# Performance work log

Hardware: AMD Instinct MI355X
Metric: run time of the kernel (lower is better)

## Reference

```python
import jax, jax.numpy as jnp
import numpy as np

B, D = 4096, 1024

def setup_inputs() -> dict:
    key = jax.random.key(0)
    k1, k2, k3 = jax.random.split(key, 3)
    # q, p are row-stochastic probability distributions (original calls q.log())
    q = jax.nn.softmax(jax.random.normal(k1, (B, D), dtype=jnp.float32), axis=-1)
    p = jax.nn.softmax(jax.random.normal(k2, (B, D), dtype=jnp.float32), axis=-1)
    # binary same-class indicator matrix
    labels_matrix = jax.random.randint(k3, (B, B), 0, 2).astype(jnp.float32)
    return {"q": q, "p": p, "labels_matrix": labels_matrix}

def reference(q, p, labels_matrix):
    d = q.shape[1]
    log_q = jnp.log(q)
    log_p = jnp.log(p)
    # torch kl_div(log_q, p) = p * (log p - log q); mean over feature dim -> [B]
    kl_div = jnp.mean(p * (log_p - log_q), axis=1)
    # pairwise kl_dis[i, j] = mean_d p[j,d] * (log p[j,d] - log q[i,d])
    # = (sum_d p[j] log p[j] - (log_q @ p^T)[i, j]) / D  -- single GEMM, no BxBxD tensor
    p_entropy_term = jnp.sum(p * log_p, axis=1)          # [B]
    cross = log_q @ p.T                                   # [B, B]
    kl_dis = (p_entropy_term[None, :] - cross) / d        # [B, B]
    # original detaches kl_dis via .cpu().numpy()
    kl_dis = jax.lax.stop_gradient(kl_dis)
    positive = kl_div + jnp.sum(kl_dis * labels_matrix, axis=1)
    negative = jnp.sum(kl_dis * (1.0 - labels_matrix), axis=1)
    return jnp.sum(positive / negative)
```

## Files before the change

kernel.cpp:

```cpp
#include <hip/hip_runtime.h>
#include <hip/hip_bf16.h>
#include <stdint.h>

#define BROWS 4096
#define DDIM  1024

typedef __bf16 bf16_t;
typedef __bf16 bf16x8 __attribute__((ext_vector_type(8)));
typedef float  f32x4  __attribute__((ext_vector_type(4)));

__device__ __forceinline__ unsigned short f2bf_bits(float f) {
    union { float f; unsigned int u; } v; v.f = f;
    unsigned int u = v.u;
    unsigned int r = (u + 0x7fffu + ((u >> 16) & 1u)) >> 16;
    return (unsigned short)r;
}

__global__ __launch_bounds__(256) void prep_kernel(
    const float* __restrict__ q, const float* __restrict__ p,
    bf16_t* __restrict__ lqb, bf16_t* __restrict__ pb,
    float* __restrict__ e, float* __restrict__ kld)
{
    const int row = blockIdx.x;
    const int t   = threadIdx.x;
    const float4* q4 = (const float4*)(q + (size_t)row * DDIM);
    const float4* p4 = (const float4*)(p + (size_t)row * DDIM);
    float4 qv = q4[t];
    float4 pv = p4[t];

    float lq0 = __logf(qv.x), lq1 = __logf(qv.y), lq2 = __logf(qv.z), lq3 = __logf(qv.w);
    float lp0 = __logf(pv.x), lp1 = __logf(pv.y), lp2 = __logf(pv.z), lp3 = __logf(pv.w);

    float esum = pv.x * lp0 + pv.y * lp1 + pv.z * lp2 + pv.w * lp3;
    float ksum = pv.x * (lp0 - lq0) + pv.y * (lp1 - lq1)
               + pv.z * (lp2 - lq2) + pv.w * (lp3 - lq3);

    ushort4 uq, up;
    uq.x = f2bf_bits(lq0); uq.y = f2bf_bits(lq1); uq.z = f2bf_bits(lq2); uq.w = f2bf_bits(lq3);
    up.x = f2bf_bits(pv.x); up.y = f2bf_bits(pv.y); up.z = f2bf_bits(pv.z); up.w = f2bf_bits(pv.w);
    ((ushort4*)(lqb + (size_t)row * DDIM))[t] = uq;
    ((ushort4*)(pb  + (size_t)row * DDIM))[t] = up;

    #pragma unroll
    for (int off = 32; off > 0; off >>= 1) {
        esum += __shfl_down(esum, off);
        ksum += __shfl_down(ksum, off);
    }
    __shared__ float se[4], sk[4];
    const int wv = t >> 6, ln = t & 63;
    if (ln == 0) { se[wv] = esum; sk[wv] = ksum; }
    __syncthreads();
    if (t == 0) {
        e[row]   = se[0] + se[1] + se[2] + se[3];
        kld[row] = (sk[0] + sk[1] + sk[2] + sk[3]) * (1.0f / DDIM);
    }
}

__global__ __launch_bounds__(256) void gemm_epi_kernel(
    const bf16_t* __restrict__ Abf,
    const bf16_t* __restrict__ Bbf,
    const float*  __restrict__ L,
    const float*  __restrict__ e,
    float* __restrict__ CS, float* __restrict__ CL, float* __restrict__ EL)
{
    __shared__ bf16_t As[128 * 32];
    __shared__ bf16_t Bs[128 * 32];

    const int t    = threadIdx.x;
    const int i0   = blockIdx.y * 128;
    const int j0   = blockIdx.x * 128;
    const int wave = t >> 6;
    const int lane = t & 63;
    const int q4   = lane >> 4;
    const int ln   = lane & 15;
    const int wrow = wave >> 1;
    const int wcol = wave & 1;

    f32x4 acc[4][4];
    #pragma unroll
    for (int a = 0; a < 4; a++)
        #pragma unroll
        for (int b = 0; b < 4; b++)
            acc[a][b] = (f32x4){0.f, 0.f, 0.f, 0.f};

    const int off0 = t * 8;
    const int off1 = (t + 256) * 8;
    const int r0 = off0 >> 5, c0 = off0 & 31;
    const int r1 = off1 >> 5, c1 = off1 & 31;

    for (int k0 = 0; k0 < DDIM; k0 += 32) {
        const bf16_t* gA0 = Abf + (size_t)(i0 + r0) * DDIM + k0 + c0;
        const bf16_t* gA1 = Abf + (size_t)(i0 + r1) * DDIM + k0 + c1;
        const bf16_t* gB0 = Bbf + (size_t)(j0 + r0) * DDIM + k0 + c0;
        const bf16_t* gB1 = Bbf + (size_t)(j0 + r1) * DDIM + k0 + c1;
        __builtin_amdgcn_global_load_lds(
            (const __attribute__((address_space(1))) void*)gA0,
            (__attribute__((address_space(3))) void*)(As + off0), 16, 0, 0);
        __builtin_amdgcn_global_load_lds(
            (const __attribute__((address_space(1))) void*)gA1,
            (__attribute__((address_space(3))) void*)(As + off1), 16, 0, 0);
        __builtin_amdgcn_global_load_lds(
            (const __attribute__((address_space(1))) void*)gB0,
            (__attribute__((address_space(3))) void*)(Bs + off0), 16, 0, 0);
        __builtin_amdgcn_global_load_lds(
            (const __attribute__((address_space(1))) void*)gB1,
            (__attribute__((address_space(3))) void*)(Bs + off1), 16, 0, 0);
        __syncthreads();

        bf16x8 af[4], bfr[4];
        #pragma unroll
        for (int mi = 0; mi < 4; mi++)
            af[mi] = *(const bf16x8*)(As + (wrow * 64 + mi * 16 + ln) * 32 + q4 * 8);
        #pragma unroll
        for (int ni = 0; ni < 4; ni++)
            bfr[ni] = *(const bf16x8*)(Bs + (wcol * 64 + ni * 16 + ln) * 32 + q4 * 8);
        #pragma unroll
        for (int mi = 0; mi < 4; mi++)
            #pragma unroll
            for (int ni = 0; ni < 4; ni++)
                acc[mi][ni] = __builtin_amdgcn_mfma_f32_16x16x32_bf16(
                    af[mi], bfr[ni], acc[mi][ni], 0, 0, 0);
        __syncthreads();
    }

    const int i_base = i0 + wrow * 64;
    const int j_base = j0 + wcol * 64;

    float e_j[4];
    #pragma unroll
    for (int ni = 0; ni < 4; ni++) e_j[ni] = e[j_base + ni * 16 + ln];

    #pragma unroll
    for (int mi = 0; mi < 4; mi++) {
        #pragma unroll
        for (int r = 0; r < 4; r++) {
            const int i = i_base + mi * 16 + q4 * 4 + r;
            const float* Lrow = L + (size_t)i * BROWS + j_base;
            float cs = 0.f, cl = 0.f, el = 0.f;
            #pragma unroll
            for (int ni = 0; ni < 4; ni++) {
                float c  = acc[mi][ni][r];
                float Lv = Lrow[ni * 16 + ln];
                cs += c;
                cl += c * Lv;
                el += e_j[ni] * Lv;
            }
            #pragma unroll
            for (int s = 1; s < 16; s <<= 1) {
                cs += __shfl_xor(cs, s);
                cl += __shfl_xor(cl, s);
                el += __shfl_xor(el, s);
            }
            if (ln == 0) {
                atomicAdd(&CS[i], cs);
                atomicAdd(&CL[i], cl);
                atomicAdd(&EL[i], el);
            }
        }
    }
}

__global__ __launch_bounds__(256) void final_kernel(
    const float* __restrict__ e, const float* __restrict__ kld,
    const float* __restrict__ CS, const float* __restrict__ CL,
    const float* __restrict__ EL, float* __restrict__ out)
{
    __shared__ float sred[4];
    __shared__ float sEtot;
    const int t = threadIdx.x;

    float s = 0.f;
    for (int j = t; j < BROWS; j += 256) s += e[j];
    #pragma unroll
    for (int off = 32; off > 0; off >>= 1) s += __shfl_down(s, off);
    if ((t & 63) == 0) sred[t >> 6] = s;
    __syncthreads();
    if (t == 0) sEtot = sred[0] + sred[1] + sred[2] + sred[3];
    __syncthreads();
    const float Etot = sEtot;
    const float invD = 1.0f / DDIM;

    float rs = 0.f;
    for (int i = t; i < BROWS; i += 256) {
        float el = EL[i], cl = CL[i], cs = CS[i];
        float pos = kld[i] + (el - cl) * invD;
        float neg = (Etot - el - cs + cl) * invD;
        rs += pos / neg;
    }
    __syncthreads();
    #pragma unroll
    for (int off = 32; off > 0; off >>= 1) rs += __shfl_down(rs, off);
    if ((t & 63) == 0) sred[t >> 6] = rs;
    __syncthreads();
    if (t == 0) out[0] = sred[0] + sred[1] + sred[2] + sred[3];
}

extern "C" void kernel_launch(void* const* d_in, const int* in_sizes, int n_in,
                              void* d_out, int out_size, void* d_ws, size_t ws_size,
                              hipStream_t stream)
{
    const float* q = (const float*)d_in[0];
    const float* p = (const float*)d_in[1];
    const float* L = (const float*)d_in[2];
    float* out = (float*)d_out;

    char* ws = (char*)d_ws;
    bf16_t* lqb = (bf16_t*)ws;
    bf16_t* pb  = (bf16_t*)(ws + (size_t)BROWS * DDIM * 2);
    float*  e   = (float*)(ws + (size_t)BROWS * DDIM * 4);
    float*  kld = e + BROWS;
    float*  CS  = kld + BROWS;
    float*  CL  = CS + BROWS;
    float*  EL  = CL + BROWS;

    hipMemsetAsync(CS, 0, 3 * BROWS * sizeof(float), stream);

    prep_kernel<<<BROWS, 256, 0, stream>>>(q, p, lqb, pb, e, kld);

    dim3 grid(BROWS / 128, BROWS / 128);
    gemm_epi_kernel<<<grid, 256, 0, stream>>>(lqb, pb, L, e, CS, CL, EL);

    final_kernel<<<1, 256, 0, stream>>>(e, kld, CS, CL, EL, out);
}
```

Before: 194.8 us.

## Double-buffer GEMM LDS tiles, fold accumulator zeroing into prep, nontemporal label loads

The GEMM main loop now uses two LDS buffers per operand and issues the next k-slice's global-to-LDS loads before computing on the current slice. This is meant to overlap memory latency with MFMA work, at the cost of doubling shared memory per block, which may lower occupancy. The separate memset of the atomic accumulators is replaced by zeroing inside the prep kernel, removing one launch. The labels matrix is also read with nontemporal loads so the large single-use stream does not pollute the cache.

```diff
diff --git a/kernel.cpp b/kernel.cpp
--- a/kernel.cpp
+++ b/kernel.cpp
@@ -19,7 +19,8 @@
 __global__ __launch_bounds__(256) void prep_kernel(
     const float* __restrict__ q, const float* __restrict__ p,
     bf16_t* __restrict__ lqb, bf16_t* __restrict__ pb,
-    float* __restrict__ e, float* __restrict__ kld)
+    float* __restrict__ e, float* __restrict__ kld,
+    float* __restrict__ CS, float* __restrict__ CL, float* __restrict__ EL)
 {
     const int row = blockIdx.x;
     const int t   = threadIdx.x;
@@ -41,6 +42,8 @@
     ((ushort4*)(lqb + (size_t)row * DDIM))[t] = uq;
     ((ushort4*)(pb  + (size_t)row * DDIM))[t] = up;
 
+    if (t == 0) { CS[row] = 0.f; CL[row] = 0.f; EL[row] = 0.f; }
+
     #pragma unroll
     for (int off = 32; off > 0; off >>= 1) {
         esum += __shfl_down(esum, off);
@@ -63,8 +66,8 @@
     const float*  __restrict__ e,
     float* __restrict__ CS, float* __restrict__ CL, float* __restrict__ EL)
 {
-    __shared__ bf16_t As[128 * 32];
-    __shared__ bf16_t Bs[128 * 32];
+    __shared__ bf16_t As[2][128 * 32];
+    __shared__ bf16_t Bs[2][128 * 32];
 
     const int t    = threadIdx.x;
     const int i0   = blockIdx.y * 128;
@@ -84,42 +87,53 @@
             acc[a][b] = (f32x4){0.f, 0.f, 0.f, 0.f};
 
     const int off0 = t * 8;
-    const int off1 = (t + 256) * 8;
+    const int off1 = off0 + 2048;
     const int r0 = off0 >> 5, c0 = off0 & 31;
     const int r1 = off1 >> 5, c1 = off1 & 31;
 
-    for (int k0 = 0; k0 < DDIM; k0 += 32) {
-        const bf16_t* gA0 = Abf + (size_t)(i0 + r0) * DDIM + k0 + c0;
-        const bf16_t* gA1 = Abf + (size_t)(i0 + r1) * DDIM + k0 + c1;
-        const bf16_t* gB0 = Bbf + (size_t)(j0 + r0) * DDIM + k0 + c0;
-        const bf16_t* gB1 = Bbf + (size_t)(j0 + r1) * DDIM + k0 + c1;
-        __builtin_amdgcn_global_load_lds(
-            (const __attribute__((address_space(1))) void*)gA0,
-            (__attribute__((address_space(3))) void*)(As + off0), 16, 0, 0);
-        __builtin_amdgcn_global_load_lds(
-            (const __attribute__((address_space(1))) void*)gA1,
-            (__attribute__((address_space(3))) void*)(As + off1), 16, 0, 0);
-        __builtin_amdgcn_global_load_lds(
-            (const __attribute__((address_space(1))) void*)gB0,
-            (__attribute__((address_space(3))) void*)(Bs + off0), 16, 0, 0);
-        __builtin_amdgcn_global_load_lds(
-            (const __attribute__((address_space(1))) void*)gB1,
-            (__attribute__((address_space(3))) void*)(Bs + off1), 16, 0, 0);
-        __syncthreads();
+    const bf16_t* gA0 = Abf + (size_t)(i0 + r0) * DDIM + c0;
+    const bf16_t* gA1 = Abf + (size_t)(i0 + r1) * DDIM + c1;
+    const bf16_t* gB0 = Bbf + (size_t)(j0 + r0) * DDIM + c0;
+    const bf16_t* gB1 = Bbf + (size_t)(j0 + r1) * DDIM + c1;
+
+    auto stage = [&](int k0, int buf) {
+        __builtin_amdgcn_global_load_lds(
+            (const __attribute__((address_space(1))) void*)(gA0 + k0),
+            (__attribute__((address_space(3))) void*)(&As[buf][off0]), 16, 0, 0);
+        __builtin_amdgcn_global_load_lds(
+            (const __attribute__((address_space(1))) void*)(gA1 + k0),
+            (__attribute__((address_space(3))) void*)(&As[buf][off1]), 16, 0, 0);
+        __builtin_amdgcn_global_load_lds(
+            (const __attribute__((address_space(1))) void*)(gB0 + k0),
+            (__attribute__((address_space(3))) void*)(&Bs[buf][off0]), 16, 0, 0);
+        __builtin_amdgcn_global_load_lds(
+            (const __attribute__((address_space(1))) void*)(gB1 + k0),
+            (__attribute__((address_space(3))) void*)(&Bs[buf][off1]), 16, 0, 0);
+    };
+
+    stage(0, 0);
+    __syncthreads();
+
+    #pragma unroll 1
+    for (int it = 0; it < DDIM / 32; ++it) {
+        const int cur = it & 1;
+        const int knext = (it + 1) * 32;
+        if (knext < DDIM) stage(knext, cur ^ 1);
 
         bf16x8 af[4], bfr[4];
         #pragma unroll
         for (int mi = 0; mi < 4; mi++)
-            af[mi] = *(const bf16x8*)(As + (wrow * 64 + mi * 16 + ln) * 32 + q4 * 8);
+            af[mi] = *(const bf16x8*)(&As[cur][(wrow * 64 + mi * 16 + ln) * 32 + q4 * 8]);
         #pragma unroll
         for (int ni = 0; ni < 4; ni++)
-            bfr[ni] = *(const bf16x8*)(Bs + (wcol * 64 + ni * 16 + ln) * 32 + q4 * 8);
+            bfr[ni] = *(const bf16x8*)(&Bs[cur][(wcol * 64 + ni * 16 + ln) * 32 + q4 * 8]);
         #pragma unroll
         for (int mi = 0; mi < 4; mi++)
             #pragma unroll
             for (int ni = 0; ni < 4; ni++)
                 acc[mi][ni] = __builtin_amdgcn_mfma_f32_16x16x32_bf16(
                     af[mi], bfr[ni], acc[mi][ni], 0, 0, 0);
+
         __syncthreads();
     }
 
@@ -140,7 +154,7 @@
             #pragma unroll
             for (int ni = 0; ni < 4; ni++) {
                 float c  = acc[mi][ni][r];
-                float Lv = Lrow[ni * 16 + ln];
+                float Lv = __builtin_nontemporal_load(Lrow + ni * 16 + ln);
                 cs += c;
                 cl += c * Lv;
                 el += e_j[ni] * Lv;
@@ -213,9 +227,7 @@
     float*  CL  = CS + BROWS;
     float*  EL  = CL + BROWS;
 
-    hipMemsetAsync(CS, 0, 3 * BROWS * sizeof(float), stream);
-
-    prep_kernel<<<BROWS, 256, 0, stream>>>(q, p, lqb, pb, e, kld);
+    prep_kernel<<<BROWS, 256, 0, stream>>>(q, p, lqb, pb, e, kld, CS, CL, EL);
 
     dim3 grid(BROWS / 128, BROWS / 128);
     gemm_epi_kernel<<<grid, 256, 0, stream>>>(lqb, pb, L, e, CS, CL, EL);
```

Result: no change. 194.2 us (-0.3%).

## Bit-pack label matrix in prep and use single-wave 64x64 GEMM tiles

Applied to the files above, without the earlier changes.

The prep kernel now reads the float label matrix once and packs each row into 64-bit ballot masks. It also zeroes the accumulators, so the separate memset is gone. The GEMM epilogue reads these compact masks and applies them with branches instead of strided float loads and multiplies. The GEMM is restructured into single-wave blocks with 64x64 tiles and no block barriers. This gives more blocks but more redundant A/B tile loads, and it relies on the labels being exactly 0/1 and on the wave-level ordering of the async global-to-LDS loads.

```diff
diff --git a/kernel.cpp b/kernel.cpp
--- a/kernel.cpp
+++ b/kernel.cpp
@@ -18,11 +18,16 @@
 
 __global__ __launch_bounds__(256) void prep_kernel(
     const float* __restrict__ q, const float* __restrict__ p,
+    const float* __restrict__ L,
     bf16_t* __restrict__ lqb, bf16_t* __restrict__ pb,
-    float* __restrict__ e, float* __restrict__ kld)
+    uint64_t* __restrict__ Lb,
+    float* __restrict__ e, float* __restrict__ kld,
+    float* __restrict__ CS, float* __restrict__ CL, float* __restrict__ EL)
 {
     const int row = blockIdx.x;
     const int t   = threadIdx.x;
+    const int wv  = t >> 6, ln = t & 63;
+
     const float4* q4 = (const float4*)(q + (size_t)row * DDIM);
     const float4* p4 = (const float4*)(p + (size_t)row * DDIM);
     float4 qv = q4[t];
@@ -41,13 +46,22 @@
     ((ushort4*)(lqb + (size_t)row * DDIM))[t] = uq;
     ((ushort4*)(pb  + (size_t)row * DDIM))[t] = up;
 
+    const float* Lrow = L + (size_t)row * BROWS;
+    #pragma unroll
+    for (int c = 0; c < 16; c++) {
+        float v = Lrow[c * 256 + t];
+        unsigned long long m = __ballot(v != 0.0f);
+        if (ln == 0) Lb[(size_t)row * 64 + c * 4 + wv] = m;
+    }
+
+    if (t == 0) { CS[row] = 0.f; CL[row] = 0.f; EL[row] = 0.f; }
+
     #pragma unroll
     for (int off = 32; off > 0; off >>= 1) {
         esum += __shfl_down(esum, off);
         ksum += __shfl_down(ksum, off);
     }
     __shared__ float se[4], sk[4];
-    const int wv = t >> 6, ln = t & 63;
     if (ln == 0) { se[wv] = esum; sk[wv] = ksum; }
     __syncthreads();
     if (t == 0) {
@@ -56,25 +70,21 @@
     }
 }
 
-__global__ __launch_bounds__(256) void gemm_epi_kernel(
+__global__ __launch_bounds__(64, 4) void gemm_epi_kernel(
     const bf16_t* __restrict__ Abf,
     const bf16_t* __restrict__ Bbf,
-    const float*  __restrict__ L,
+    const uint64_t* __restrict__ Lb,
     const float*  __restrict__ e,
     float* __restrict__ CS, float* __restrict__ CL, float* __restrict__ EL)
 {
-    __shared__ bf16_t As[128 * 32];
-    __shared__ bf16_t Bs[128 * 32];
-
-    const int t    = threadIdx.x;
-    const int i0   = blockIdx.y * 128;
-    const int j0   = blockIdx.x * 128;
-    const int wave = t >> 6;
-    const int lane = t & 63;
+    __shared__ bf16_t As[64 * 32];
+    __shared__ bf16_t Bs[64 * 32];
+
+    const int lane = threadIdx.x;
+    const int i0   = blockIdx.y * 64;
+    const int j0   = blockIdx.x * 64;
     const int q4   = lane >> 4;
     const int ln   = lane & 15;
-    const int wrow = wave >> 1;
-    const int wcol = wave & 1;
 
     f32x4 acc[4][4];
     #pragma unroll
@@ -83,67 +93,64 @@
         for (int b = 0; b < 4; b++)
             acc[a][b] = (f32x4){0.f, 0.f, 0.f, 0.f};
 
-    const int off0 = t * 8;
-    const int off1 = (t + 256) * 8;
-    const int r0 = off0 >> 5, c0 = off0 & 31;
-    const int r1 = off1 >> 5, c1 = off1 & 31;
-
+    const bf16_t* gA[4];
+    const bf16_t* gB[4];
+    int ldsoff[4];
+    #pragma unroll
+    for (int n = 0; n < 4; n++) {
+        const int c = n * 64 + lane;
+        const int r = c >> 2;
+        const int col = (c & 3) * 8;
+        gA[n] = Abf + (size_t)(i0 + r) * DDIM + col;
+        gB[n] = Bbf + (size_t)(j0 + r) * DDIM + col;
+        ldsoff[n] = c * 8;
+    }
+
+    #pragma unroll 1
     for (int k0 = 0; k0 < DDIM; k0 += 32) {
-        const bf16_t* gA0 = Abf + (size_t)(i0 + r0) * DDIM + k0 + c0;
-        const bf16_t* gA1 = Abf + (size_t)(i0 + r1) * DDIM + k0 + c1;
-        const bf16_t* gB0 = Bbf + (size_t)(j0 + r0) * DDIM + k0 + c0;
-        const bf16_t* gB1 = Bbf + (size_t)(j0 + r1) * DDIM + k0 + c1;
-        __builtin_amdgcn_global_load_lds(
-            (const __attribute__((address_space(1))) void*)gA0,
-            (__attribute__((address_space(3))) void*)(As + off0), 16, 0, 0);
-        __builtin_amdgcn_global_load_lds(
-            (const __attribute__((address_space(1))) void*)gA1,
-            (__attribute__((address_space(3))) void*)(As + off1), 16, 0, 0);
-        __builtin_amdgcn_global_load_lds(
-            (const __attribute__((address_space(1))) void*)gB0,
-            (__attribute__((address_space(3))) void*)(Bs + off0), 16, 0, 0);
-        __builtin_amdgcn_global_load_lds(
-            (const __attribute__((address_space(1))) void*)gB1,
-            (__attribute__((address_space(3))) void*)(Bs + off1), 16, 0, 0);
-        __syncthreads();
+        #pragma unroll
+        for (int n = 0; n < 4; n++)
+            __builtin_amdgcn_global_load_lds(
+                (const __attribute__((address_space(1))) void*)(gA[n] + k0),
+                (__attribute__((address_space(3))) void*)(As + ldsoff[n]), 16, 0, 0);
+        #pragma unroll
+        for (int n = 0; n < 4; n++)
+            __builtin_amdgcn_global_load_lds(
+                (const __attribute__((address_space(1))) void*)(gB[n] + k0),
+                (__attribute__((address_space(3))) void*)(Bs + ldsoff[n]), 16, 0, 0);
 
         bf16x8 af[4], bfr[4];
         #pragma unroll
         for (int mi = 0; mi < 4; mi++)
-            af[mi] = *(const bf16x8*)(As + (wrow * 64 + mi * 16 + ln) * 32 + q4 * 8);
+            af[mi] = *(const bf16x8*)(As + (mi * 16 + ln) * 32 + q4 * 8);
         #pragma unroll
         for (int ni = 0; ni < 4; ni++)
-            bfr[ni] = *(const bf16x8*)(Bs + (wcol * 64 + ni * 16 + ln) * 32 + q4 * 8);
+            bfr[ni] = *(const bf16x8*)(Bs + (ni * 16 + ln) * 32 + q4 * 8);
         #pragma unroll
         for (int mi = 0; mi < 4; mi++)
             #pragma unroll
             for (int ni = 0; ni < 4; ni++)
                 acc[mi][ni] = __builtin_amdgcn_mfma_f32_16x16x32_bf16(
                     af[mi], bfr[ni], acc[mi][ni], 0, 0, 0);
-        __syncthreads();
-    }
-
-    const int i_base = i0 + wrow * 64;
-    const int j_base = j0 + wcol * 64;
+    }
 
     float e_j[4];
     #pragma unroll
-    for (int ni = 0; ni < 4; ni++) e_j[ni] = e[j_base + ni * 16 + ln];
+    for (int ni = 0; ni < 4; ni++) e_j[ni] = e[j0 + ni * 16 + ln];
 
     #pragma unroll
     for (int mi = 0; mi < 4; mi++) {
         #pragma unroll
         for (int r = 0; r < 4; r++) {
-            const int i = i_base + mi * 16 + q4 * 4 + r;
-            const float* Lrow = L + (size_t)i * BROWS + j_base;
+            const int i = i0 + mi * 16 + q4 * 4 + r;
+            const uint64_t m  = Lb[(size_t)i * 64 + (j0 >> 6)];
+            const uint64_t ms = m >> ln;
             float cs = 0.f, cl = 0.f, el = 0.f;
             #pragma unroll
             for (int ni = 0; ni < 4; ni++) {
-                float c  = acc[mi][ni][r];
-                float Lv = Lrow[ni * 16 + ln];
+                float c = acc[mi][ni][r];
                 cs += c;
-                cl += c * Lv;
-                el += e_j[ni] * Lv;
+                if ((ms >> (ni * 16)) & 1ull) { cl += c; el += e_j[ni]; }
             }
             #pragma unroll
             for (int s = 1; s < 16; s <<= 1) {
@@ -212,13 +219,12 @@
     float*  CS  = kld + BROWS;
     float*  CL  = CS + BROWS;
     float*  EL  = CL + BROWS;
-
-    hipMemsetAsync(CS, 0, 3 * BROWS * sizeof(float), stream);
-
-    prep_kernel<<<BROWS, 256, 0, stream>>>(q, p, lqb, pb, e, kld);
-
-    dim3 grid(BROWS / 128, BROWS / 128);
-    gemm_epi_kernel<<<grid, 256, 0, stream>>>(lqb, pb, L, e, CS, CL, EL);
+    uint64_t* Lb = (uint64_t*)(EL + BROWS);
+
+    prep_kernel<<<BROWS, 256, 0, stream>>>(q, p, L, lqb, pb, Lb, e, kld, CS, CL, EL);
+
+    dim3 grid(BROWS / 64, BROWS / 64);
+    gemm_epi_kernel<<<grid, 64, 0, stream>>>(lqb, pb, Lb, e, CS, CL, EL);
 
     final_kernel<<<1, 256, 0, stream>>>(e, kld, CS, CL, EL, out);
 }
```

Measured after the change: 214.8 us. 1.1x slower.
